# Kernel tuning notes

Hardware: AMD Instinct MI355X
Metric: run time of the kernel (lower is better)

## Reference

```python
import jax, jax.numpy as jnp
import numpy as np

N, Dx, Dt, M, K = 524288, 128, 64, 32, 8
SK, SS = 1.0, 1.0  # l2 regularization strengths (experts, gate)


def setup_inputs() -> dict:
    key = jax.random.key(0)
    ks = jax.random.split(key, 6)
    w = 0.02  # small weight scale keeps per-sample log-likelihoods in fp32 range
    return {
        "x": jax.random.normal(ks[0], (N, Dx), dtype=jnp.float32),
        "t": jax.random.normal(ks[1], (N, Dt), dtype=jnp.float32),
        "y": jax.random.normal(ks[2], (N, M), dtype=jnp.float32),
        "Wm": jax.random.normal(ks[3], (K, Dx, M), dtype=jnp.float32) * w,
        "bm": jnp.zeros((K, M), dtype=jnp.float32),
        "Wv": jax.random.normal(ks[4], (K, Dx, M), dtype=jnp.float32) * w,
        "bv": jnp.zeros((K, M), dtype=jnp.float32),
        "Wg": jax.random.normal(ks[5], (Dt, K), dtype=jnp.float32) * w,
        "bg": jnp.zeros((K,), dtype=jnp.float32),
    }


def reference(x, t, y, Wm, bm, Wv, bv, Wg, bg):
    # Gate: softmax Dense over t -> pi [N, K]
    pi = jax.nn.softmax(t @ Wg + bg, axis=1)
    # All K expert heads as one batched matmul (fused form of the Python loop)
    mean = jnp.einsum("nd,kdm->nkm", x, Wm) + bm      # [N, K, M]
    logvar = jnp.einsum("nd,kdm->nkm", x, Wv) + bv    # [N, K, M]
    half_log_2pi = 0.5 * jnp.float32(np.log(2.0 * np.pi))
    diff = y[:, None, :] - mean                        # [N, K, M]
    # Gaussian log-likelihood per sample per expert -> [N, K]
    ll = -jnp.sum(diff * diff / (2.0 * jnp.exp(logvar)) + half_log_2pi + 0.5 * logvar, axis=2)
    # Mixture likelihood, then NLL (matches original: sum_k pi_k * exp(ll_k))
    mix = jnp.sum(pi * jnp.exp(ll), axis=1)            # [N]
    # Keras l1_l2(l2=s) kernel regularizers (biases excluded)
    reg = SK * (jnp.sum(Wm * Wm) + jnp.sum(Wv * Wv)) + SS * jnp.sum(Wg * Wg)
    return -jnp.sum(jnp.log(mix)) + reg
```

## Files before the change

kernel.cpp:

```cpp
#include <hip/hip_runtime.h>
#include <hip/hip_bf16.h>


#define NN 524288
#define DX 128
#define DT 64
#define MDIM 32
#define KEXP 8
#define TILE_R 32
#define THREADS 1024
#define GRID_MAIN 512
#define TPB 32

typedef __bf16 bf16x8 __attribute__((ext_vector_type(8)));
typedef float f32x4 __attribute__((ext_vector_type(4)));
typedef long long i64;

__device__ __forceinline__ bf16x8 cvt8(const f32x4 a, const f32x4 b) {
  bf16x8 r;
  r[0] = (__bf16)a[0]; r[1] = (__bf16)a[1]; r[2] = (__bf16)a[2]; r[3] = (__bf16)a[3];
  r[4] = (__bf16)b[0]; r[5] = (__bf16)b[1]; r[6] = (__bf16)b[2]; r[7] = (__bf16)b[3];
  return r;
}
__device__ __forceinline__ i64 cvt8f8(const f32x4 a, const f32x4 b) {
  int p0 = __builtin_amdgcn_cvt_pk_fp8_f32(a[0], a[1], 0, 0);
  p0 = __builtin_amdgcn_cvt_pk_fp8_f32(a[2], a[3], p0, 1);
  int p1 = __builtin_amdgcn_cvt_pk_fp8_f32(b[0], b[1], 0, 0);
  p1 = __builtin_amdgcn_cvt_pk_fp8_f32(b[2], b[3], p1, 1);
  return (i64)(((unsigned long long)(unsigned)p1 << 32) | (unsigned)p0);
}

#define MFMA16(a, b, c) __builtin_amdgcn_mfma_f32_16x16x32_bf16(a, b, c, 0, 0, 0)
#define MFMA8(a, b, c)  __builtin_amdgcn_mfma_f32_16x16x32_fp8_fp8(a, b, c, 0, 0, 0)

#define B_LDS() do { \
  asm volatile("s_waitcnt lgkmcnt(0)" ::: "memory"); \
  __builtin_amdgcn_s_barrier(); \
  __builtin_amdgcn_sched_barrier(0); } while (0)

#define HL2PI 0.91893853320467274f

__global__ __launch_bounds__(THREADS, 4) void mdn_main(
    const float* __restrict__ x, const float* __restrict__ t,
    const float* __restrict__ y, const float* __restrict__ Wm,
    const float* __restrict__ bm, const float* __restrict__ Wv,
    const float* __restrict__ bv, const float* __restrict__ Wg,
    const float* __restrict__ bg, float* __restrict__ partials,
    float* __restrict__ out_atomic)
{
  __shared__ __align__(16) unsigned char  xs_l[2][TILE_R * DX];
  __shared__ __align__(16) unsigned short ts_l[2][TILE_R * DT];
  __shared__ __align__(16) float ys_l[2][TILE_R * MDIM];
  __shared__ __align__(16) unsigned short wg_lds[2 * 64 * 8];
  __shared__ __align__(16) float llp4[2][TILE_R * 68];
  __shared__ __align__(16) float glog[2][TILE_R * 8];
  __shared__ float red_s[16];

  const int tid = threadIdx.x;
  const int lane = tid & 63;
  const int wv = tid >> 6;
  const int l15 = lane & 15;
  const int lhi = lane >> 4;
  const int kx = wv & 7;
  const int hh = wv >> 3;

  int st_ldsoff;
  const float* st_base;
  int st_stride;
  if (tid < 512) {
    const int r = tid >> 4, s = tid & 15, g = s ^ (r & 7);
    st_base = x + (size_t)r * DX + g * 8;
    st_stride = TILE_R * DX;
    st_ldsoff = r * 128 + s * 8;
  } else if (tid < 768) {
    const int u = tid - 512, r = u >> 3, s = u & 7, g = s ^ (r & 7);
    st_base = t + (size_t)r * DT + g * 8;
    st_stride = TILE_R * DT;
    st_ldsoff = r * 128 + s * 16;
  } else {
    const int u = tid - 768, r = u >> 3, s = u & 7, g = s ^ (r & 7);
    st_base = y + (size_t)r * MDIM + g * 4;
    st_stride = TILE_R * MDIM;
    st_ldsoff = r * 128 + s * 16;
  }

  f32x4 sa, sb;
  auto issue = [&](int tile) {
    const float* p = st_base + (size_t)tile * st_stride;
    sa = *(const f32x4*)p;
    if (tid < 768) sb = *(const f32x4*)(p + 4);
  };
  auto commit = [&](int buf) {
    if (tid < 512)      *(i64*)((char*)xs_l[buf] + st_ldsoff) = cvt8f8(sa, sb);
    else if (tid < 768) *(bf16x8*)((char*)ts_l[buf] + st_ldsoff) = cvt8(sa, sb);
    else                *(f32x4*)((char*)ys_l[buf] + st_ldsoff) = sa;
  };

  const int first = blockIdx.x * TPB;
  issue(first);

  const f32x4 bmean = *(const f32x4*)&bm[kx * MDIM + hh * 16 + lhi * 4];
  const f32x4 blv   = *(const f32x4*)&bv[kx * MDIM + hh * 16 + lhi * 4];
  f32x4 bgv = {0.f, 0.f, 0.f, 0.f};
  if (wv < 2) bgv = *(const f32x4*)&bg[(lhi & 1) * 4];

  i64 bfrag[2][4];
  #pragma unroll
  for (int ct = 0; ct < 2; ++ct) {
    const float* W = (ct ? Wv : Wm) + (size_t)kx * (DX * MDIM);
    const int mcol = hh * 16 + l15;
    #pragma unroll
    for (int kk = 0; kk < 4; ++kk) {
      f32x4 wa, wb;
      #pragma unroll
      for (int i = 0; i < 4; ++i) {
        wa[i] = W[(kk * 32 + lhi * 8 + i) * MDIM + mcol];
        wb[i] = W[(kk * 32 + lhi * 8 + 4 + i) * MDIM + mcol];
      }
      bfrag[ct][kk] = cvt8f8(wa, wb);
    }
  }
  if (wv == 15) {
    #pragma unroll
    for (int kk = 0; kk < 2; ++kk) {
      bf16x8 tmp;
      #pragma unroll
      for (int i = 0; i < 8; ++i) {
        const int d = kk * 32 + lhi * 8 + i;
        tmp[i] = (__bf16)((l15 < KEXP) ? Wg[d * KEXP + l15] : 0.f);
      }
      *(bf16x8*)((char*)wg_lds + (kk * 64 + lane) * 16) = tmp;
    }
  }

  commit(0);
  B_LDS();

  float loss_acc = 0.f;

  auto do_lse = [&](int pb) {
    const int rr = (wv - 4) * 16 + l15;
    const f32x4 lgv = *(const f32x4*)&glog[pb][rr * 8 + (lhi & 1) * 4];
    const int kb = (lhi & 1) * 4;
    f32x4 a4;
    #pragma unroll
    for (int j = 0; j < 4; ++j) {
      const f32x4 pA = *(const f32x4*)&llp4[pb][rr * 68 + (kb + j) * 4];
      const f32x4 pB = *(const f32x4*)&llp4[pb][rr * 68 + 32 + (kb + j) * 4];
      const float s8 = pA[0] + pA[1] + pA[2] + pA[3]
                     + pB[0] + pB[1] + pB[2] + pB[3];
      a4[j] = lgv[j] - s8 - 32.0f * HL2PI;
    }
    float mg = fmaxf(fmaxf(lgv[0], lgv[1]), fmaxf(lgv[2], lgv[3]));
    float ma = fmaxf(fmaxf(a4[0], a4[1]), fmaxf(a4[2], a4[3]));
    mg = fmaxf(mg, __shfl_xor(mg, 16));
    ma = fmaxf(ma, __shfl_xor(ma, 16));
    float eg = __expf(lgv[0] - mg) + __expf(lgv[1] - mg)
             + __expf(lgv[2] - mg) + __expf(lgv[3] - mg);
    float ea = __expf(a4[0] - ma) + __expf(a4[1] - ma)
             + __expf(a4[2] - ma) + __expf(a4[3] - ma);
    eg += __shfl_xor(eg, 16);
    ea += __shfl_xor(ea, 16);
    if (lhi == 0)
      loss_acc += (mg + __logf(eg)) - (ma + __logf(ea));
  };

  for (int it = 0; it < TPB; ++it) {
    const int cur = it & 1;
    issue(first + ((it + 1 < TPB) ? it + 1 : it));

    if (it && (wv == 4 || wv == 5)) do_lse(cur ^ 1);

    if (wv < 2) {
      const int rr = wv * 16 + l15;
      const int r7 = rr & 7;
      f32x4 g = {0.f, 0.f, 0.f, 0.f};
      #pragma unroll
      for (int kk = 0; kk < 2; ++kk) {
        const int s = (kk * 4 + lhi) ^ r7;
        const bf16x8 tf = *(const bf16x8*)((const char*)ts_l[cur] + rr * 128 + s * 16);
        const bf16x8 wf = *(const bf16x8*)((const char*)wg_lds + (kk * 64 + lane) * 16);
        g = MFMA16(wf, tf, g);
      }
      if (lhi < 2) {
        f32x4 lg;
        #pragma unroll
        for (int j = 0; j < 4; ++j) lg[j] = g[j] + bgv[j];
        *(f32x4*)&glog[cur][rr * 8 + lhi * 4] = lg;
      }
    }

    const unsigned char* xc = xs_l[cur];
    const float* yc = ys_l[cur];
    #pragma unroll
    for (int rt = 0; rt < 2; ++rt) {
      const int rr = rt * 16 + l15;
      const int r7 = rr & 7;
      f32x4 acc0 = bmean, acc1 = blv;
      #pragma unroll
      for (int kk = 0; kk < 4; ++kk) {
        const int s = (kk * 4 + lhi) ^ r7;
        const i64 af = *(const i64*)(xc + rr * 128 + s * 8);
        acc0 = MFMA8(bfrag[0][kk], af, acc0);
        acc1 = MFMA8(bfrag[1][kk], af, acc1);
      }
      const int sy = (hh * 4 + lhi) ^ r7;
      const f32x4 y4 = *(const f32x4*)&yc[rr * 32 + sy * 4];
      float part = 0.f;
      #pragma unroll
      for (int j = 0; j < 4; ++j) {
        const float d = y4[j] - acc0[j];
        part += d * d * (0.5f * __expf(-acc1[j])) + 0.5f * acc1[j];
      }
      llp4[cur][rr * 68 + hh * 32 + kx * 4 + lhi] = part;
    }

    commit(cur ^ 1);
    B_LDS();
  }
  if (wv == 4 || wv == 5) do_lse((TPB - 1) & 1);

  loss_acc += __shfl_xor(loss_acc, 1);
  loss_acc += __shfl_xor(loss_acc, 2);
  loss_acc += __shfl_xor(loss_acc, 4);
  loss_acc += __shfl_xor(loss_acc, 8);
  loss_acc += __shfl_xor(loss_acc, 16);
  loss_acc += __shfl_xor(loss_acc, 32);
  if (lane == 0) red_s[wv] = loss_acc;
  __syncthreads();
  if (tid == 0) {
    float s = 0.f;
    #pragma unroll
    for (int w = 0; w < 16; ++w) s += red_s[w];
    if (partials) partials[blockIdx.x] = s;
    else atomicAdd(out_atomic, s);
  }
}

__global__ void mdn_reg(const float* __restrict__ Wm, const float* __restrict__ Wv,
                        const float* __restrict__ Wg, float* __restrict__ partials,
                        float* __restrict__ out_atomic)
{
  __shared__ float red[4];
  const int gid = blockIdx.x * 256 + threadIdx.x;
  const int stride = 64 * 256;
  float s = 0.f;
  for (int i = gid; i < DX * MDIM * KEXP; i += stride) { float w = Wm[i]; s += w * w; }
  for (int i = gid; i < DX * MDIM * KEXP; i += stride) { float w = Wv[i]; s += w * w; }
  for (int i = gid; i < DT * KEXP; i += stride)        { float w = Wg[i]; s += w * w; }
  s += __shfl_xor(s, 1);
  s += __shfl_xor(s, 2);
  s += __shfl_xor(s, 4);
  s += __shfl_xor(s, 8);
  s += __shfl_xor(s, 16);
  s += __shfl_xor(s, 32);
  if ((threadIdx.x & 63) == 0) red[threadIdx.x >> 6] = s;
  __syncthreads();
  if (threadIdx.x == 0) {
    float b = red[0] + red[1] + red[2] + red[3];
    if (partials) partials[GRID_MAIN + blockIdx.x] = b;
    else atomicAdd(out_atomic, b);
  }
}

__global__ void mdn_final(const float* __restrict__ partials, float* __restrict__ out)
{
  __shared__ float red[4];
  float s = 0.f;
  for (int i = threadIdx.x; i < GRID_MAIN + 64; i += 256) s += partials[i];
  s += __shfl_xor(s, 1);
  s += __shfl_xor(s, 2);
  s += __shfl_xor(s, 4);
  s += __shfl_xor(s, 8);
  s += __shfl_xor(s, 16);
  s += __shfl_xor(s, 32);
  if ((threadIdx.x & 63) == 0) red[threadIdx.x >> 6] = s;
  __syncthreads();
  if (threadIdx.x == 0) out[0] = red[0] + red[1] + red[2] + red[3];
}

extern "C" void kernel_launch(void* const* d_in, const int* in_sizes, int n_in,
                              void* d_out, int out_size, void* d_ws, size_t ws_size,
                              hipStream_t stream)
{
  const float* x  = (const float*)d_in[0];
  const float* t  = (const float*)d_in[1];
  const float* y  = (const float*)d_in[2];
  const float* Wm = (const float*)d_in[3];
  const float* bm = (const float*)d_in[4];
  const float* Wv = (const float*)d_in[5];
  const float* bv = (const float*)d_in[6];
  const float* Wg = (const float*)d_in[7];
  const float* bg = (const float*)d_in[8];
  float* out = (float*)d_out;

  if (ws_size >= (GRID_MAIN + 64) * sizeof(float)) {
    float* partials = (float*)d_ws;
    mdn_main<<<GRID_MAIN, THREADS, 0, stream>>>(x, t, y, Wm, bm, Wv, bv, Wg, bg,
                                                partials, nullptr);
    mdn_reg<<<64, 256, 0, stream>>>(Wm, Wv, Wg, partials, nullptr);
    mdn_final<<<1, 256, 0, stream>>>(partials, out);
  } else {
    hipMemsetAsync(out, 0, sizeof(float), stream);
    mdn_main<<<GRID_MAIN, THREADS, 0, stream>>>(x, t, y, Wm, bm, Wv, bv, Wg, bg,
                                                nullptr, out);
    mdn_reg<<<64, 256, 0, stream>>>(Wm, Wv, Wg, nullptr, out);
  }
}
```

Before: 114.5 us.

## Double row tile to 64 and halve tiles per block

Each pipeline step now handles 64 rows instead of 32, with half as many steps per block. All 1024 threads load x, while t and y loads are split across the thread halves. Gate and log-sum-exp work is spread over four waves each. The aim is to cut per-tile barrier and loop overhead and get more memory traffic in flight per step, at the cost of more LDS and registers per block, which may lower occupancy.

Measured after the change: 120.5 us. 5.2% more time.

```diff
diff --git a/kernel.cpp b/kernel.cpp
--- a/kernel.cpp
+++ b/kernel.cpp
@@ -7,10 +7,10 @@
 #define DT 64
 #define MDIM 32
 #define KEXP 8
-#define TILE_R 32
+#define TILE_R 64
 #define THREADS 1024
 #define GRID_MAIN 512
-#define TPB 32
+#define TPB 16
 
 typedef __bf16 bf16x8 __attribute__((ext_vector_type(8)));
 typedef float f32x4 __attribute__((ext_vector_type(4)));
@@ -64,36 +64,34 @@
   const int kx = wv & 7;
   const int hh = wv >> 3;
 
-  int st_ldsoff;
-  const float* st_base;
-  int st_stride;
-  if (tid < 512) {
-    const int r = tid >> 4, s = tid & 15, g = s ^ (r & 7);
-    st_base = x + (size_t)r * DX + g * 8;
-    st_stride = TILE_R * DX;
-    st_ldsoff = r * 128 + s * 8;
-  } else if (tid < 768) {
-    const int u = tid - 512, r = u >> 3, s = u & 7, g = s ^ (r & 7);
-    st_base = t + (size_t)r * DT + g * 8;
-    st_stride = TILE_R * DT;
-    st_ldsoff = r * 128 + s * 16;
-  } else {
-    const int u = tid - 768, r = u >> 3, s = u & 7, g = s ^ (r & 7);
-    st_base = y + (size_t)r * MDIM + g * 4;
-    st_stride = TILE_R * MDIM;
-    st_ldsoff = r * 128 + s * 16;
-  }
-
-  f32x4 sa, sb;
+  const int xr = tid >> 4, xsl = tid & 15;
+  const int x_src = xr * DX + ((xsl ^ (xr & 7)) << 3);
+  const int x_dst = xr * 128 + (xsl << 3);
+  const int tr = tid >> 3, tsl = tid & 7;
+  const int t_src = tr * DT + ((tsl ^ (tr & 7)) << 3);
+  const int t_dst = tr * 128 + (tsl << 4);
+  const int uy = tid - 512;
+  const int yr = uy >> 3, ysl = uy & 7;
+  const int y_src = yr * MDIM + ((ysl ^ (yr & 7)) << 2);
+  const int y_dst = yr * 128 + (ysl << 4);
+
+  f32x4 sa, sb, ea, eb;
   auto issue = [&](int tile) {
-    const float* p = st_base + (size_t)tile * st_stride;
-    sa = *(const f32x4*)p;
-    if (tid < 768) sb = *(const f32x4*)(p + 4);
+    const float* xp = x + (size_t)tile * (TILE_R * DX) + x_src;
+    sa = *(const f32x4*)xp;
+    sb = *(const f32x4*)(xp + 4);
+    if (tid < 512) {
+      const float* tp = t + (size_t)tile * (TILE_R * DT) + t_src;
+      ea = *(const f32x4*)tp;
+      eb = *(const f32x4*)(tp + 4);
+    } else {
+      ea = *(const f32x4*)(y + (size_t)tile * (TILE_R * MDIM) + y_src);
+    }
   };
   auto commit = [&](int buf) {
-    if (tid < 512)      *(i64*)((char*)xs_l[buf] + st_ldsoff) = cvt8f8(sa, sb);
-    else if (tid < 768) *(bf16x8*)((char*)ts_l[buf] + st_ldsoff) = cvt8(sa, sb);
-    else                *(f32x4*)((char*)ys_l[buf] + st_ldsoff) = sa;
+    *(i64*)((char*)xs_l[buf] + x_dst) = cvt8f8(sa, sb);
+    if (tid < 512) *(bf16x8*)((char*)ts_l[buf] + t_dst) = cvt8(ea, eb);
+    else           *(f32x4*)((char*)ys_l[buf] + y_dst) = ea;
   };
 
   const int first = blockIdx.x * TPB;
@@ -102,7 +100,7 @@
   const f32x4 bmean = *(const f32x4*)&bm[kx * MDIM + hh * 16 + lhi * 4];
   const f32x4 blv   = *(const f32x4*)&bv[kx * MDIM + hh * 16 + lhi * 4];
   f32x4 bgv = {0.f, 0.f, 0.f, 0.f};
-  if (wv < 2) bgv = *(const f32x4*)&bg[(lhi & 1) * 4];
+  if (wv < 4) bgv = *(const f32x4*)&bg[(lhi & 1) * 4];
 
   i64 bfrag[2][4];
   #pragma unroll
@@ -157,21 +155,21 @@
     ma = fmaxf(ma, __shfl_xor(ma, 16));
     float eg = __expf(lgv[0] - mg) + __expf(lgv[1] - mg)
              + __expf(lgv[2] - mg) + __expf(lgv[3] - mg);
-    float ea = __expf(a4[0] - ma) + __expf(a4[1] - ma)
-             + __expf(a4[2] - ma) + __expf(a4[3] - ma);
+    float ea2 = __expf(a4[0] - ma) + __expf(a4[1] - ma)
+              + __expf(a4[2] - ma) + __expf(a4[3] - ma);
     eg += __shfl_xor(eg, 16);
-    ea += __shfl_xor(ea, 16);
+    ea2 += __shfl_xor(ea2, 16);
     if (lhi == 0)
-      loss_acc += (mg + __logf(eg)) - (ma + __logf(ea));
+      loss_acc += (mg + __logf(eg)) - (ma + __logf(ea2));
   };
 
   for (int it = 0; it < TPB; ++it) {
     const int cur = it & 1;
     issue(first + ((it + 1 < TPB) ? it + 1 : it));
 
-    if (it && (wv == 4 || wv == 5)) do_lse(cur ^ 1);
-
-    if (wv < 2) {
+    if (it && wv >= 4 && wv < 8) do_lse(cur ^ 1);
+
+    if (wv < 4) {
       const int rr = wv * 16 + l15;
       const int r7 = rr & 7;
       f32x4 g = {0.f, 0.f, 0.f, 0.f};
@@ -193,7 +191,7 @@
     const unsigned char* xc = xs_l[cur];
     const float* yc = ys_l[cur];
     #pragma unroll
-    for (int rt = 0; rt < 2; ++rt) {
+    for (int rt = 0; rt < 4; ++rt) {
       const int rr = rt * 16 + l15;
       const int r7 = rr & 7;
       f32x4 acc0 = bmean, acc1 = blv;
@@ -218,7 +216,7 @@
     commit(cur ^ 1);
     B_LDS();
   }
-  if (wv == 4 || wv == 5) do_lse((TPB - 1) & 1);
+  if (wv >= 4 && wv < 8) do_lse((TPB - 1) & 1);
 
   loss_acc += __shfl_xor(loss_acc, 1);
   loss_acc += __shfl_xor(loss_acc, 2);
```

## Repartition expert waves to cover all M columns for half the row tile

Applied to the files above, without the earlier changes.

Each wave now holds weight fragments for both 16-column halves of its expert and handles one 16-row half of the tile, where before it held one column half and looped over both row halves. Each wave's partial already covers all 32 outputs, so the llp4 reduction buffer shrinks and the LSE step reads one f32x4 per expert instead of two. Expert biases are staged into shared memory and loaded per tile instead of living in registers. Each wave holds twice as many weight fragments, which raises register pressure, while the number of MFMAs per wave stays the same.

New measurement: 176.4 us. 54.1% more time.

```diff
diff --git a/kernel.cpp b/kernel.cpp
--- a/kernel.cpp
+++ b/kernel.cpp
@@ -52,7 +52,9 @@
   __shared__ __align__(16) unsigned short ts_l[2][TILE_R * DT];
   __shared__ __align__(16) float ys_l[2][TILE_R * MDIM];
   __shared__ __align__(16) unsigned short wg_lds[2 * 64 * 8];
-  __shared__ __align__(16) float llp4[2][TILE_R * 68];
+  __shared__ __align__(16) float bm_s[KEXP * MDIM];
+  __shared__ __align__(16) float bv_s[KEXP * MDIM];
+  __shared__ __align__(16) float llp4[2][TILE_R * 40];
   __shared__ __align__(16) float glog[2][TILE_R * 8];
   __shared__ float red_s[16];
 
@@ -62,7 +64,7 @@
   const int l15 = lane & 15;
   const int lhi = lane >> 4;
   const int kx = wv & 7;
-  const int hh = wv >> 3;
+  const int sh = wv >> 3;
 
   int st_ldsoff;
   const float* st_base;
@@ -99,25 +101,28 @@
   const int first = blockIdx.x * TPB;
   issue(first);
 
-  const f32x4 bmean = *(const f32x4*)&bm[kx * MDIM + hh * 16 + lhi * 4];
-  const f32x4 blv   = *(const f32x4*)&bv[kx * MDIM + hh * 16 + lhi * 4];
+  if (tid < KEXP * MDIM) bm_s[tid] = bm[tid];
+  else if (tid < 2 * KEXP * MDIM) bv_s[tid - KEXP * MDIM] = bv[tid - KEXP * MDIM];
   f32x4 bgv = {0.f, 0.f, 0.f, 0.f};
   if (wv < 2) bgv = *(const f32x4*)&bg[(lhi & 1) * 4];
 
-  i64 bfrag[2][4];
+  i64 bfrag[2][2][4];
   #pragma unroll
   for (int ct = 0; ct < 2; ++ct) {
     const float* W = (ct ? Wv : Wm) + (size_t)kx * (DX * MDIM);
-    const int mcol = hh * 16 + l15;
     #pragma unroll
-    for (int kk = 0; kk < 4; ++kk) {
-      f32x4 wa, wb;
-      #pragma unroll
-      for (int i = 0; i < 4; ++i) {
-        wa[i] = W[(kk * 32 + lhi * 8 + i) * MDIM + mcol];
-        wb[i] = W[(kk * 32 + lhi * 8 + 4 + i) * MDIM + mcol];
-      }
-      bfrag[ct][kk] = cvt8f8(wa, wb);
+    for (int hh = 0; hh < 2; ++hh) {
+      const int mcol = hh * 16 + l15;
+      #pragma unroll
+      for (int kk = 0; kk < 4; ++kk) {
+        f32x4 wa, wb;
+        #pragma unroll
+        for (int i = 0; i < 4; ++i) {
+          wa[i] = W[(kk * 32 + lhi * 8 + i) * MDIM + mcol];
+          wb[i] = W[(kk * 32 + lhi * 8 + 4 + i) * MDIM + mcol];
+        }
+        bfrag[ct][hh][kk] = cvt8f8(wa, wb);
+      }
     }
   }
   if (wv == 15) {
@@ -145,11 +150,8 @@
     f32x4 a4;
     #pragma unroll
     for (int j = 0; j < 4; ++j) {
-      const f32x4 pA = *(const f32x4*)&llp4[pb][rr * 68 + (kb + j) * 4];
-      const f32x4 pB = *(const f32x4*)&llp4[pb][rr * 68 + 32 + (kb + j) * 4];
-      const float s8 = pA[0] + pA[1] + pA[2] + pA[3]
-                     + pB[0] + pB[1] + pB[2] + pB[3];
-      a4[j] = lgv[j] - s8 - 32.0f * HL2PI;
+      const f32x4 pq = *(const f32x4*)&llp4[pb][rr * 40 + (kb + j) * 4];
+      a4[j] = lgv[j] - (pq[0] + pq[1] + pq[2] + pq[3]) - 32.0f * HL2PI;
     }
     float mg = fmaxf(fmaxf(lgv[0], lgv[1]), fmaxf(lgv[2], lgv[3]));
     float ma = fmaxf(fmaxf(a4[0], a4[1]), fmaxf(a4[2], a4[3]));
@@ -157,12 +159,12 @@
     ma = fmaxf(ma, __shfl_xor(ma, 16));
     float eg = __expf(lgv[0] - mg) + __expf(lgv[1] - mg)
              + __expf(lgv[2] - mg) + __expf(lgv[3] - mg);
-    float ea = __expf(a4[0] - ma) + __expf(a4[1] - ma)
-             + __expf(a4[2] - ma) + __expf(a4[3] - ma);
+    float ea2 = __expf(a4[0] - ma) + __expf(a4[1] - ma)
+              + __expf(a4[2] - ma) + __expf(a4[3] - ma);
     eg += __shfl_xor(eg, 16);
-    ea += __shfl_xor(ea, 16);
+    ea2 += __shfl_xor(ea2, 16);
     if (lhi == 0)
-      loss_acc += (mg + __logf(eg)) - (ma + __logf(ea));
+      loss_acc += (mg + __logf(eg)) - (ma + __logf(ea2));
   };
 
   for (int it = 0; it < TPB; ++it) {
@@ -190,29 +192,36 @@
       }
     }
 
-    const unsigned char* xc = xs_l[cur];
-    const float* yc = ys_l[cur];
-    #pragma unroll
-    for (int rt = 0; rt < 2; ++rt) {
-      const int rr = rt * 16 + l15;
+    {
+      const unsigned char* xc = xs_l[cur];
+      const float* yc = ys_l[cur];
+      const int rr = sh * 16 + l15;
       const int r7 = rr & 7;
-      f32x4 acc0 = bmean, acc1 = blv;
+      f32x4 am0 = *(const f32x4*)&bm_s[kx * MDIM + lhi * 4];
+      f32x4 am1 = *(const f32x4*)&bm_s[kx * MDIM + 16 + lhi * 4];
+      f32x4 av0 = *(const f32x4*)&bv_s[kx * MDIM + lhi * 4];
+      f32x4 av1 = *(const f32x4*)&bv_s[kx * MDIM + 16 + lhi * 4];
       #pragma unroll
       for (int kk = 0; kk < 4; ++kk) {
         const int s = (kk * 4 + lhi) ^ r7;
         const i64 af = *(const i64*)(xc + rr * 128 + s * 8);
-        acc0 = MFMA8(bfrag[0][kk], af, acc0);
-        acc1 = MFMA8(bfrag[1][kk], af, acc1);
-      }
-      const int sy = (hh * 4 + lhi) ^ r7;
-      const f32x4 y4 = *(const f32x4*)&yc[rr * 32 + sy * 4];
+        am0 = MFMA8(bfrag[0][0][kk], af, am0);
+        am1 = MFMA8(bfrag[0][1][kk], af, am1);
+        av0 = MFMA8(bfrag[1][0][kk], af, av0);
+        av1 = MFMA8(bfrag[1][1][kk], af, av1);
+      }
+      const int s0 = lhi ^ r7, s1 = (4 + lhi) ^ r7;
+      const f32x4 y0v = *(const f32x4*)&yc[rr * 32 + s0 * 4];
+      const f32x4 y1v = *(const f32x4*)&yc[rr * 32 + s1 * 4];
       float part = 0.f;
       #pragma unroll
       for (int j = 0; j < 4; ++j) {
-        const float d = y4[j] - acc0[j];
-        part += d * d * (0.5f * __expf(-acc1[j])) + 0.5f * acc1[j];
-      }
-      llp4[cur][rr * 68 + hh * 32 + kx * 4 + lhi] = part;
+        const float d0 = y0v[j] - am0[j];
+        const float d1 = y1v[j] - am1[j];
+        part += d0 * d0 * (0.5f * __expf(-av0[j])) + 0.5f * av0[j];
+        part += d1 * d1 * (0.5f * __expf(-av1[j])) + 0.5f * av1[j];
+      }
+      llp4[cur][rr * 40 + kx * 4 + lhi] = part;
     }
 
     commit(cur ^ 1);
```
